# Kernel tuning notes

Measured on AMD Instinct MI355X. Metric: run time of the kernel, lower is better.

## Reference

```python
import jax, jax.numpy as jnp
import numpy as np

STEP = 0.5     # config.saxs_loss.step (Angstrom bin width of P(r) grid)
DMAX = 100.0   # config.saxs_loss.dmax (max pairwise distance considered)
NBINS = int(DMAX / STEP) + 1  # 201 r-bins
N_RES = 256
N_ATOM = 37


def _compute_saxs(all_atom_pos, all_atom_mask):
    """Differentiable pair-distance distribution P(r) on grid r_k = k*STEP.

    Pairwise distances between all masked atoms are soft-binned (linear
    interpolation between the two neighboring bins, which keeps gradients
    w.r.t. coordinates) and the histogram is normalized to sum to 1.
    """
    x = all_atom_pos.reshape(-1, 3)          # [N, 3], N = N_res*37
    m = all_atom_mask.reshape(-1)            # [N]
    n = x.shape[0]
    # Pairwise distances via Gram trick (avoids [N,N,3] intermediate).
    sq = jnp.sum(x * x, axis=-1)             # [N]
    d2 = sq[:, None] + sq[None, :] - 2.0 * (x @ x.T)   # [N, N]
    d = jnp.sqrt(jnp.maximum(d2, 1e-12))
    # Pair weights: both atoms present, exclude self-pairs.
    w = m[:, None] * m[None, :]
    w = w * (1.0 - jnp.eye(n, dtype=w.dtype))
    # Soft linear binning onto the r-grid (differentiable through frac).
    t = jnp.clip(d / STEP, 0.0, NBINS - 1.000001)
    lo = jnp.floor(t).astype(jnp.int32)
    frac = t - lo.astype(d.dtype)
    hist = jnp.zeros((NBINS,), dtype=d.dtype)
    hist = hist.at[lo.ravel()].add((w * (1.0 - frac)).ravel())
    hist = hist.at[jnp.minimum(lo + 1, NBINS - 1).ravel()].add((w * frac).ravel())
    return hist / (jnp.sum(hist) + 1e-12)


def setup_inputs() -> dict:
    key = jax.random.key(0)
    k1, k2, k3 = jax.random.split(key, 3)
    # True structure: coordinates spread over ~tens of Angstroms.
    true_pos = jax.random.normal(k1, (N_RES, N_ATOM, 3), dtype=jnp.float32) * 10.0
    # Predicted structure: true + small perturbation.
    pred_pos = true_pos + jax.random.normal(k2, (N_RES, N_ATOM, 3), dtype=jnp.float32) * 0.5
    mask = jnp.ones((N_RES, N_ATOM), dtype=jnp.float32)
    return {
        "final_atom_positions": pred_pos,
        "all_atom_positions": true_pos,
        "all_atom_mask": mask,
    }


def reference(final_atom_positions, all_atom_positions, all_atom_mask):
    pred_saxs = _compute_saxs(final_atom_positions, all_atom_mask)
    true_saxs = _compute_saxs(all_atom_positions, all_atom_mask)
    # torch.nn.L1Loss(reduction='sum')
    return jnp.sum(jnp.abs(pred_saxs - true_saxs))
```

## Files before the change

kernel.cpp:

```cpp
#include <hip/hip_runtime.h>


#define TILE    256
#define NTILES  37
#define TPAIRS  (NTILES * (NTILES + 1) / 2)
#define NBINS   201
#define NREP    32
#define RSTRIDE 201
#define HSTRIDE 256
#define QSCALE  256.0f

template<bool DIAG>
__device__ __forceinline__ void accum_tile(
    const float* __restrict__ pos, const float* __restrict__ mask,
    int aBase, int t, int lane,
    float xj, float yj, float zj, unsigned vj,
    unsigned int* __restrict__ rep)
{
    #pragma unroll
    for (int c = 0; c < 4; ++c) {
        const int ia = aBase + c * 64 + lane;
        const int cx = __float_as_int(2.0f * pos[3 * ia]);
        const int cy = __float_as_int(2.0f * pos[3 * ia + 1]);
        const int cz = __float_as_int(2.0f * pos[3 * ia + 2]);
        const int cmi = (int)(mask[ia] * QSCALE);

        #pragma unroll 4
        for (int i = 0; i < 64; ++i) {
            const float sx = __int_as_float(__builtin_amdgcn_readlane(cx, i));
            const float sy = __int_as_float(__builtin_amdgcn_readlane(cy, i));
            const float sz = __int_as_float(__builtin_amdgcn_readlane(cz, i));
            const unsigned smi = (unsigned)__builtin_amdgcn_readlane(cmi, i);

            const float dx = sx - xj;
            const float dy = sy - yj;
            const float dz = sz - zj;
            const float d2 = fmaf(dx, dx, fmaf(dy, dy, dz * dz));
            const float tt = fminf(__builtin_amdgcn_sqrtf(d2), 200.0f);
            const unsigned lo   = (unsigned)tt;
            const float    frac = __builtin_amdgcn_fractf(tt);
            unsigned tot = smi & vj;
            if (DIAG) tot = (c * 64 + i < t) ? tot : 0u;
            const float    wpf = (float)tot;
            const unsigned q   = (unsigned)fmaf(wpf, frac, 0.5f);
            const unsigned pack = (q << 16) + (tot - q);
            atomicAdd(&rep[lo], pack);
        }
    }
}

__global__ __launch_bounds__(TILE) void saxs_hist_kernel(
    const float* __restrict__ posPred,
    const float* __restrict__ posTrue,
    const float* __restrict__ mask,
    unsigned long long* __restrict__ gh,
    unsigned int* __restrict__ counter,
    float* __restrict__ out)
{
    const int t    = threadIdx.x;
    const int lane = t & 63;
    const int s    = blockIdx.y;
    const float* __restrict__ pos = s ? posTrue : posPred;
    unsigned long long* __restrict__ ghist = gh + s * HSTRIDE;

    int p = blockIdx.x;
    int a = 0;
    while (p >= NTILES - a) { p -= NTILES - a; ++a; }
    const int b = a + p;

    __shared__ unsigned int sHist[NREP * RSTRIDE];
    for (int k = t; k < NREP * RSTRIDE; k += TILE) sHist[k] = 0u;

    const int jg = b * TILE + t;
    const float xj = 2.0f * pos[3 * jg];
    const float yj = 2.0f * pos[3 * jg + 1];
    const float zj = 2.0f * pos[3 * jg + 2];
    const unsigned vj = (mask[jg] != 0.0f) ? 0xFFFFFFFFu : 0u;

    __syncthreads();

    unsigned int* __restrict__ rep = sHist + (t & (NREP - 1)) * RSTRIDE;

    if (a != b) accum_tile<false>(pos, mask, a * TILE, t, lane, xj, yj, zj, vj, rep);
    else        accum_tile<true >(pos, mask, a * TILE, t, lane, xj, yj, zj, vj, rep);

    __syncthreads();

    for (int k = t; k < NBINS; k += TILE) {
        unsigned int acc = 0;
        #pragma unroll
        for (int r = 0; r < NREP; ++r) {
            acc += sHist[r * RSTRIDE + k] & 0xFFFFu;
            if (k > 0) acc += sHist[r * RSTRIDE + k - 1] >> 16;
        }
        atomicAdd(&ghist[k], (unsigned long long)acc);
    }

    __syncthreads();
    __shared__ int sLast;
    if (t == 0) {
        __threadfence();
        const unsigned prev = __hip_atomic_fetch_add(
            counter, 1u, __ATOMIC_ACQ_REL, __HIP_MEMORY_SCOPE_AGENT);
        sLast = (prev == 2u * TPAIRS - 1u);
    }
    __syncthreads();
    if (sLast && t < 64) {
        const int ln = t;
        float hp[4], ht[4];
        float sp = 0.0f, st = 0.0f;
        #pragma unroll
        for (int r = 0; r < 4; ++r) {
            const int k = ln + 64 * r;
            float av = 0.0f, cv = 0.0f;
            if (k < NBINS) {
                av = (float)__hip_atomic_load(&gh[k],           __ATOMIC_RELAXED,
                                              __HIP_MEMORY_SCOPE_AGENT);
                cv = (float)__hip_atomic_load(&gh[HSTRIDE + k], __ATOMIC_RELAXED,
                                              __HIP_MEMORY_SCOPE_AGENT);
            }
            hp[r] = av; ht[r] = cv;
            sp += av; st += cv;
        }
        #pragma unroll
        for (int off = 32; off > 0; off >>= 1) {
            sp += __shfl_xor(sp, off);
            st += __shfl_xor(st, off);
        }
        sp += 1e-12f;
        st += 1e-12f;
        float l = 0.0f;
        #pragma unroll
        for (int r = 0; r < 4; ++r) l += fabsf(hp[r] / sp - ht[r] / st);
        #pragma unroll
        for (int off = 32; off > 0; off >>= 1) l += __shfl_xor(l, off);
        if (ln == 0) out[0] = l;
    }
}

extern "C" void kernel_launch(void* const* d_in, const int* in_sizes, int n_in,
                              void* d_out, int out_size, void* d_ws, size_t ws_size,
                              hipStream_t stream)
{
    const float* pred = (const float*)d_in[0];
    const float* tru  = (const float*)d_in[1];
    const float* msk  = (const float*)d_in[2];
    float* out = (float*)d_out;
    unsigned long long* ws = (unsigned long long*)d_ws;
    unsigned int* counter = (unsigned int*)(ws + 2 * HSTRIDE);

    hipMemsetAsync(d_ws, 0, (2 * HSTRIDE + 1) * sizeof(unsigned long long), stream);

    dim3 grid(TPAIRS, 2);
    saxs_hist_kernel<<<grid, dim3(TILE), 0, stream>>>(pred, tru, msk, ws, counter, out);
}
```

Measured before the change: 140.0 us.

## Fuse pred and true histograms into one block per tile pair

Each block now computes pairwise distances for both the predicted and true structures, sharing the mask, diagonal logic and tile indexing, and halving the grid from two planes to one. Shared histogram replicas per structure are cut from 32 to 16 so both histograms fit in LDS. This amortises the per-block setup, clearing and reduction and doubles independent work per thread, at the cost of more atomic contention per replica, higher register pressure, and fewer blocks to spread across CUs.

```diff
diff --git a/kernel.cpp b/kernel.cpp
--- a/kernel.cpp
+++ b/kernel.cpp
@@ -5,46 +5,65 @@
 #define NTILES  37
 #define TPAIRS  (NTILES * (NTILES + 1) / 2)
 #define NBINS   201
-#define NREP    32
+#define NREP    16
 #define RSTRIDE 201
+#define SOFF    (NREP * RSTRIDE)
 #define HSTRIDE 256
 #define QSCALE  256.0f
 
 template<bool DIAG>
 __device__ __forceinline__ void accum_tile(
-    const float* __restrict__ pos, const float* __restrict__ mask,
+    const float* __restrict__ posP, const float* __restrict__ posT,
+    const float* __restrict__ mask,
     int aBase, int t, int lane,
-    float xj, float yj, float zj, unsigned vj,
-    unsigned int* __restrict__ rep)
+    float xjp, float yjp, float zjp,
+    float xjt, float yjt, float zjt, unsigned vj,
+    unsigned int* __restrict__ repP, unsigned int* __restrict__ repT)
 {
     #pragma unroll
     for (int c = 0; c < 4; ++c) {
         const int ia = aBase + c * 64 + lane;
-        const int cx = __float_as_int(2.0f * pos[3 * ia]);
-        const int cy = __float_as_int(2.0f * pos[3 * ia + 1]);
-        const int cz = __float_as_int(2.0f * pos[3 * ia + 2]);
+        const int cxp = __float_as_int(2.0f * posP[3 * ia]);
+        const int cyp = __float_as_int(2.0f * posP[3 * ia + 1]);
+        const int czp = __float_as_int(2.0f * posP[3 * ia + 2]);
+        const int cxt = __float_as_int(2.0f * posT[3 * ia]);
+        const int cyt = __float_as_int(2.0f * posT[3 * ia + 1]);
+        const int czt = __float_as_int(2.0f * posT[3 * ia + 2]);
         const int cmi = (int)(mask[ia] * QSCALE);
 
         #pragma unroll 4
         for (int i = 0; i < 64; ++i) {
-            const float sx = __int_as_float(__builtin_amdgcn_readlane(cx, i));
-            const float sy = __int_as_float(__builtin_amdgcn_readlane(cy, i));
-            const float sz = __int_as_float(__builtin_amdgcn_readlane(cz, i));
+            const float sxp = __int_as_float(__builtin_amdgcn_readlane(cxp, i));
+            const float syp = __int_as_float(__builtin_amdgcn_readlane(cyp, i));
+            const float szp = __int_as_float(__builtin_amdgcn_readlane(czp, i));
+            const float sxt = __int_as_float(__builtin_amdgcn_readlane(cxt, i));
+            const float syt = __int_as_float(__builtin_amdgcn_readlane(cyt, i));
+            const float szt = __int_as_float(__builtin_amdgcn_readlane(czt, i));
             const unsigned smi = (unsigned)__builtin_amdgcn_readlane(cmi, i);
 
-            const float dx = sx - xj;
-            const float dy = sy - yj;
-            const float dz = sz - zj;
-            const float d2 = fmaf(dx, dx, fmaf(dy, dy, dz * dz));
-            const float tt = fminf(__builtin_amdgcn_sqrtf(d2), 200.0f);
-            const unsigned lo   = (unsigned)tt;
-            const float    frac = __builtin_amdgcn_fractf(tt);
             unsigned tot = smi & vj;
             if (DIAG) tot = (c * 64 + i < t) ? tot : 0u;
-            const float    wpf = (float)tot;
-            const unsigned q   = (unsigned)fmaf(wpf, frac, 0.5f);
-            const unsigned pack = (q << 16) + (tot - q);
-            atomicAdd(&rep[lo], pack);
+            const float wpf = (float)tot;
+
+            const float dxp = sxp - xjp;
+            const float dyp = syp - yjp;
+            const float dzp = szp - zjp;
+            const float d2p = fmaf(dxp, dxp, fmaf(dyp, dyp, dzp * dzp));
+            const float ttp = fminf(__builtin_amdgcn_sqrtf(d2p), 200.0f);
+            const unsigned lop = (unsigned)ttp;
+            const float    frp = __builtin_amdgcn_fractf(ttp);
+            const unsigned qp  = (unsigned)fmaf(wpf, frp, 0.5f);
+            atomicAdd(&repP[lop], (qp << 16) + (tot - qp));
+
+            const float dxt = sxt - xjt;
+            const float dyt = syt - yjt;
+            const float dzt = szt - zjt;
+            const float d2t = fmaf(dxt, dxt, fmaf(dyt, dyt, dzt * dzt));
+            const float ttt = fminf(__builtin_amdgcn_sqrtf(d2t), 200.0f);
+            const unsigned lot = (unsigned)ttt;
+            const float    frt = __builtin_amdgcn_fractf(ttt);
+            const unsigned qt  = (unsigned)fmaf(wpf, frt, 0.5f);
+            atomicAdd(&repT[lot], (qt << 16) + (tot - qt));
         }
     }
 }
@@ -59,41 +78,47 @@
 {
     const int t    = threadIdx.x;
     const int lane = t & 63;
-    const int s    = blockIdx.y;
-    const float* __restrict__ pos = s ? posTrue : posPred;
-    unsigned long long* __restrict__ ghist = gh + s * HSTRIDE;
 
     int p = blockIdx.x;
     int a = 0;
     while (p >= NTILES - a) { p -= NTILES - a; ++a; }
     const int b = a + p;
 
-    __shared__ unsigned int sHist[NREP * RSTRIDE];
-    for (int k = t; k < NREP * RSTRIDE; k += TILE) sHist[k] = 0u;
+    __shared__ unsigned int sHist[2 * NREP * RSTRIDE];
+    for (int k = t; k < 2 * NREP * RSTRIDE; k += TILE) sHist[k] = 0u;
 
     const int jg = b * TILE + t;
-    const float xj = 2.0f * pos[3 * jg];
-    const float yj = 2.0f * pos[3 * jg + 1];
-    const float zj = 2.0f * pos[3 * jg + 2];
+    const float xjp = 2.0f * posPred[3 * jg];
+    const float yjp = 2.0f * posPred[3 * jg + 1];
+    const float zjp = 2.0f * posPred[3 * jg + 2];
+    const float xjt = 2.0f * posTrue[3 * jg];
+    const float yjt = 2.0f * posTrue[3 * jg + 1];
+    const float zjt = 2.0f * posTrue[3 * jg + 2];
     const unsigned vj = (mask[jg] != 0.0f) ? 0xFFFFFFFFu : 0u;
 
     __syncthreads();
 
-    unsigned int* __restrict__ rep = sHist + (t & (NREP - 1)) * RSTRIDE;
+    unsigned int* __restrict__ repP = sHist + (t & (NREP - 1)) * RSTRIDE;
+    unsigned int* __restrict__ repT = repP + SOFF;
 
-    if (a != b) accum_tile<false>(pos, mask, a * TILE, t, lane, xj, yj, zj, vj, rep);
-    else        accum_tile<true >(pos, mask, a * TILE, t, lane, xj, yj, zj, vj, rep);
+    if (a != b) accum_tile<false>(posPred, posTrue, mask, a * TILE, t, lane,
+                                  xjp, yjp, zjp, xjt, yjt, zjt, vj, repP, repT);
+    else        accum_tile<true >(posPred, posTrue, mask, a * TILE, t, lane,
+                                  xjp, yjp, zjp, xjt, yjt, zjt, vj, repP, repT);
 
     __syncthreads();
 
-    for (int k = t; k < NBINS; k += TILE) {
+    for (int k = t; k < 2 * NBINS; k += TILE) {
+        const int s  = (k < NBINS) ? 0 : 1;
+        const int kk = k - s * NBINS;
+        const unsigned int* h = sHist + s * SOFF;
         unsigned int acc = 0;
         #pragma unroll
         for (int r = 0; r < NREP; ++r) {
-            acc += sHist[r * RSTRIDE + k] & 0xFFFFu;
-            if (k > 0) acc += sHist[r * RSTRIDE + k - 1] >> 16;
+            acc += h[r * RSTRIDE + kk] & 0xFFFFu;
+            if (kk > 0) acc += h[r * RSTRIDE + kk - 1] >> 16;
         }
-        atomicAdd(&ghist[k], (unsigned long long)acc);
+        atomicAdd(&gh[s * HSTRIDE + kk], (unsigned long long)acc);
     }
 
     __syncthreads();
@@ -102,7 +127,7 @@
         __threadfence();
         const unsigned prev = __hip_atomic_fetch_add(
             counter, 1u, __ATOMIC_ACQ_REL, __HIP_MEMORY_SCOPE_AGENT);
-        sLast = (prev == 2u * TPAIRS - 1u);
+        sLast = (prev == TPAIRS - 1u);
     }
     __syncthreads();
     if (sLast && t < 64) {
@@ -151,6 +176,6 @@
 
     hipMemsetAsync(d_ws, 0, (2 * HSTRIDE + 1) * sizeof(unsigned long long), stream);
 
-    dim3 grid(TPAIRS, 2);
-    saxs_hist_kernel<<<grid, dim3(TILE), 0, stream>>>(pred, tru, msk, ws, counter, out);
+    saxs_hist_kernel<<<dim3(TPAIRS), dim3(TILE), 0, stream>>>(
+        pred, tru, msk, ws, counter, out);
 }
```

After: 135.4 us. 3.3% less time.
